# Kernel tuning notes

Hardware: AMD Instinct MI355X
Metric: run time of the kernel (lower is better)

The kernel has to match this reference:

```python
import math
import jax, jax.numpy as jnp
import numpy as np

B, L, D, DK = 2, 2046, 1024, 64
H, GH, LH = 16, 8, 8   # total / global / local heads
WS = 3                  # hardcoded window_size in source
MAX_VAL = 1e9


def setup_inputs() -> dict:
    key = jax.random.key(0)
    ks = jax.random.split(key, 7)
    x = jax.random.normal(ks[0], (B, L, D), dtype=jnp.float32)
    mask = jnp.ones((B, 1, L, L), dtype=jnp.float32)
    s = 0.02
    Wq = jax.random.normal(ks[1], (D, D), dtype=jnp.float32) * s   # torch Linear weight [out,in]
    bq = jnp.zeros((D,), dtype=jnp.float32)
    Wk = jax.random.normal(ks[2], (H, DK, DK), dtype=jnp.float32) * s
    bk = jnp.zeros((H, DK), dtype=jnp.float32)
    Wv = jax.random.normal(ks[3], (H, DK, DK), dtype=jnp.float32) * s
    bv = jnp.zeros((H, DK), dtype=jnp.float32)
    return {"x": x, "mask": mask, "Wq": Wq, "bq": bq,
            "Wk": Wk, "bk": bk, "Wv": Wv, "bv": bv}


def reference(x, mask, Wq, bq, Wk, bk, Wv, bv):
    b, l, d = x.shape
    scale = 1.0 / math.sqrt(DK)

    q = x @ Wq.T + bq                                   # [b,l,d]
    q = q.reshape(b, l, H, DK).transpose(0, 2, 1, 3)    # [b,h,l,dk]
    kv = x.reshape(b, l, H, DK).transpose(0, 2, 1, 3)   # k and v are both raw x

    # ---------------- global heads: full attention ----------------
    qg = q[:, :GH]                                      # [b,gh,l,dk]
    kg = kv[:, :GH]
    kgp = jnp.einsum('bhli,hoi->bhlo', kg, Wk[:GH]) + bk[:GH][None, :, None, :]
    vgp = jnp.einsum('bhli,hoi->bhlo', kg, Wv[:GH]) + bv[:GH][None, :, None, :]
    sg = jnp.einsum('bhld,bhmd->bhlm', qg, kgp) * scale  # [b,gh,l,l]
    mfull = (mask[:, 0] == 0)[:, None]                   # [b,1,l,l]
    sg = jnp.where(mfull, -MAX_VAL, sg)
    pg = jax.nn.softmax(sg, axis=-1)
    vg = jnp.einsum('bhlm,bhmd->bhld', pg, vgp)          # [b,gh,l,dk]

    # ---------------- local heads: window-pooled attention ----------------
    nw = l // WS
    ql = q[:, GH:]                                       # [b,lh,l,dk]
    kl = kv[:, GH:]
    # mean-pool keys over non-overlapping windows (pool_method='mean');
    # source uses the SAME pooled tensor for both K and V (repeat(2,...))
    kw = kl.reshape(b, LH, nw, WS, DK).mean(axis=3)      # [b,lh,nw,dk]
    # window mask: majority of window columns valid, per query row
    wm = mask[:, 0].reshape(b, l, nw, WS).sum(-1) >= math.ceil(WS / 2)  # [b,l,nw]
    klp = jnp.einsum('bhni,hoi->bhno', kw, Wk[GH:]) + bk[GH:][None, :, None, :]
    vlp = jnp.einsum('bhni,hoi->bhno', kw, Wv[GH:]) + bv[GH:][None, :, None, :]
    sl = jnp.einsum('bhld,bhnd->bhln', ql, klp) * scale  # [b,lh,l,nw]
    sl = jnp.where(~wm[:, None], -MAX_VAL, sl)
    pl = jax.nn.softmax(sl, axis=-1)
    vl = jnp.einsum('bhln,bhnd->bhld', pl, vlp)          # [b,lh,l,dk]

    value_all = jnp.concatenate([vg, vl], axis=1)        # [b,h,l,dk]
    return (value_all, pg, pl)
```

## Files before the change

kernel.cpp:

```cpp
#include <hip/hip_runtime.h>
#include <hip/hip_bf16.h>
#include <stdint.h>

typedef __bf16 bf16;
typedef bf16 bf16x8 __attribute__((ext_vector_type(8)));
typedef float f32x4 __attribute__((ext_vector_type(4)));

#define B_ 2
#define L_ 2046
#define H_ 16
#define NW_ 682
#define LP_ 2048
#define NWP_ 704
#define M_ (B_*L_)
#define SCALE_ 0.125f

__device__ inline bf16x8 zf8() {
  bf16x8 v;
#pragma unroll
  for (int e = 0; e < 8; ++e) v[e] = (bf16)0.0f;
  return v;
}

__device__ inline uint32_t pkbf(float a, float b) {
  uint16_t ua = __builtin_bit_cast(uint16_t, (bf16)a);
  uint16_t ub = __builtin_bit_cast(uint16_t, (bf16)b);
  return (uint32_t)ua | ((uint32_t)ub << 16);
}
__device__ inline float upk_lo(uint32_t u) { return __builtin_bit_cast(float, u << 16); }
__device__ inline float upk_hi(uint32_t u) { return __builtin_bit_cast(float, u & 0xffff0000u); }

__global__ __launch_bounds__(256) void cast4(const float* __restrict__ in,
                                             bf16* __restrict__ out, int n) {
  int i = (blockIdx.x * 256 + threadIdx.x) * 4;
  if (i + 3 < n) {
    float4 v = *reinterpret_cast<const float4*>(in + i);
    bf16 tmp[4];
    tmp[0] = (bf16)v.x; tmp[1] = (bf16)v.y; tmp[2] = (bf16)v.z; tmp[3] = (bf16)v.w;
    *reinterpret_cast<uint64_t*>(out + i) = *reinterpret_cast<const uint64_t*>(tmp);
  } else {
    for (; i < n; ++i) out[i] = (bf16)in[i];
  }
}

__global__ __launch_bounds__(256) void qgemm_t(const bf16* __restrict__ X,
                                               const bf16* __restrict__ W,
                                               const float* __restrict__ bq,
                                               bf16* __restrict__ Q) {
  __shared__ bf16 As[64 * 40];
  __shared__ bf16 Bs[128 * 40];
  int t = threadIdx.x, lane = t & 63, w = t >> 6;
  int lid = lane & 15, g = lane >> 4;
  int m0 = blockIdx.x * 64, n0 = blockIdx.y * 128;
  int wm = (w >> 1) * 32, wn = (w & 1) * 64;
  f32x4 z4 = {0.f, 0.f, 0.f, 0.f};
  f32x4 acc[2][4];
#pragma unroll
  for (int mi = 0; mi < 2; ++mi)
#pragma unroll
    for (int ni = 0; ni < 4; ++ni) acc[mi][ni] = z4;
  int r1 = t >> 2, c1 = t & 3;
  for (int k0 = 0; k0 < 1024; k0 += 32) {
    int ga = m0 + r1; if (ga >= M_) ga = M_ - 1;
    bf16x8 av = *reinterpret_cast<const bf16x8*>(X + (size_t)ga * 1024 + k0 + c1 * 8);
    bf16x8 bv1 = *reinterpret_cast<const bf16x8*>(W + (size_t)(n0 + r1) * 1024 + k0 + c1 * 8);
    bf16x8 bv2 = *reinterpret_cast<const bf16x8*>(W + (size_t)(n0 + 64 + r1) * 1024 + k0 + c1 * 8);
    __syncthreads();
    *reinterpret_cast<bf16x8*>(As + r1 * 40 + c1 * 8) = av;
    *reinterpret_cast<bf16x8*>(Bs + r1 * 40 + c1 * 8) = bv1;
    *reinterpret_cast<bf16x8*>(Bs + (64 + r1) * 40 + c1 * 8) = bv2;
    __syncthreads();
    bf16x8 af[2], bfr[4];
#pragma unroll
    for (int mi = 0; mi < 2; ++mi)
      af[mi] = *reinterpret_cast<const bf16x8*>(As + (wm + mi * 16 + lid) * 40 + g * 8);
#pragma unroll
    for (int ni = 0; ni < 4; ++ni)
      bfr[ni] = *reinterpret_cast<const bf16x8*>(Bs + (wn + ni * 16 + lid) * 40 + g * 8);
#pragma unroll
    for (int mi = 0; mi < 2; ++mi)
#pragma unroll
      for (int ni = 0; ni < 4; ++ni)
        acc[mi][ni] = __builtin_amdgcn_mfma_f32_16x16x32_bf16(af[mi], bfr[ni], acc[mi][ni], 0, 0, 0);
  }
  float bias[4];
#pragma unroll
  for (int ni = 0; ni < 4; ++ni) bias[ni] = bq[n0 + wn + ni * 16 + lid];
#pragma unroll
  for (int mi = 0; mi < 2; ++mi)
#pragma unroll
    for (int r = 0; r < 4; ++r) {
      int row = m0 + wm + mi * 16 + g * 4 + r;
      if (row < M_) {
#pragma unroll
        for (int ni = 0; ni < 4; ++ni)
          Q[(size_t)row * 1024 + n0 + wn + ni * 16 + lid] = (bf16)(acc[mi][ni][r] + bias[ni]);
      }
    }
}

__global__ __launch_bounds__(256) void proj_g32(const float* __restrict__ x,
    const float* __restrict__ Wk, const float* __restrict__ bk,
    const float* __restrict__ Wv, const float* __restrict__ bv,
    bf16* __restrict__ KGP, bf16* __restrict__ VGT) {
  __shared__ float xs[64][64];
  __shared__ float wks[64][65];
  __shared__ float wvs[64][65];
  int t = threadIdx.x;
  int lb = blockIdx.x, bh = blockIdx.y;
  int b = bh >> 3, h = bh & 7;
  int l0 = lb * 64;
  for (int idx = t; idx < 4096; idx += 256) {
    int r = idx >> 6, c = idx & 63;
    int l = l0 + r;
    xs[r][c] = (l < L_) ? x[((size_t)b * L_ + l) * 1024 + h * 64 + c] : 0.0f;
    wks[r][c] = Wk[(size_t)h * 4096 + idx];
    wvs[r][c] = Wv[(size_t)h * 4096 + idx];
  }
  __syncthreads();
  int o = t & 63, lg = t >> 6;
  float kbias = bk[h * 64 + o], vbias = bv[h * 64 + o];
  float vacc[16];
  const size_t outb = (size_t)bh * LP_ * 64;
  for (int ls = 0; ls < 16; ++ls) {
    int l = lg * 16 + ls;
    float ka = kbias, va = vbias;
#pragma unroll
    for (int i = 0; i < 64; ++i) {
      float xv = xs[l][i];
      ka = fmaf(xv, wks[o][i], ka);
      va = fmaf(xv, wvs[o][i], va);
    }
    KGP[outb + (size_t)(l0 + l) * 64 + o] = (bf16)ka;
    vacc[ls] = va;
  }
  __syncthreads();
#pragma unroll
  for (int ls = 0; ls < 16; ++ls) wvs[o][lg * 16 + ls] = vacc[ls];
  __syncthreads();
  for (int idx = t; idx < 4096; idx += 256) {
    int oo = idx >> 6, ll = idx & 63;
    VGT[(size_t)bh * 64 * LP_ + (size_t)oo * LP_ + l0 + ll] = (bf16)wvs[oo][ll];
  }
}

__global__ __launch_bounds__(256) void proj_l32(const float* __restrict__ x,
    const float* __restrict__ Wk, const float* __restrict__ bk,
    const float* __restrict__ Wv, const float* __restrict__ bv,
    bf16* __restrict__ KLP, bf16* __restrict__ VLT) {
  __shared__ float xs[64][64];
  __shared__ float wks[64][65];
  __shared__ float wvs[64][65];
  int t = threadIdx.x;
  int nb = blockIdx.x, bh = blockIdx.y;
  int b = bh >> 3, h = bh & 7;
  int n0 = nb * 64;
  int hh = 8 + h;
  for (int idx = t; idx < 4096; idx += 256) {
    int r = idx >> 6, c = idx & 63;
    int n = n0 + r;
    float v = 0.0f;
    if (n < NW_) {
      size_t base = ((size_t)b * L_ + 3 * n) * 1024 + hh * 64 + c;
      v = (x[base] + x[base + 1024] + x[base + 2048]) * (1.0f / 3.0f);
    }
    xs[r][c] = v;
    wks[r][c] = Wk[(size_t)hh * 4096 + idx];
    wvs[r][c] = Wv[(size_t)hh * 4096 + idx];
  }
  __syncthreads();
  int o = t & 63, lg = t >> 6;
  float kbias = bk[hh * 64 + o], vbias = bv[hh * 64 + o];
  float vacc[16];
  const size_t outb = (size_t)bh * NWP_ * 64;
  for (int ls = 0; ls < 16; ++ls) {
    int l = lg * 16 + ls;
    float ka = kbias, va = vbias;
#pragma unroll
    for (int i = 0; i < 64; ++i) {
      float xv = xs[l][i];
      ka = fmaf(xv, wks[o][i], ka);
      va = fmaf(xv, wvs[o][i], va);
    }
    KLP[outb + (size_t)(n0 + l) * 64 + o] = (bf16)ka;
    vacc[ls] = va;
  }
  __syncthreads();
#pragma unroll
  for (int ls = 0; ls < 16; ++ls) wvs[o][lg * 16 + ls] = vacc[ls];
  __syncthreads();
  for (int idx = t; idx < 4096; idx += 256) {
    int oo = idx >> 6, ll = idx & 63;
    VLT[(size_t)bh * 64 * NWP_ + (size_t)oo * NWP_ + n0 + ll] = (bf16)wvs[oo][ll];
  }
}

__global__ __launch_bounds__(256) void maskprep(const float* __restrict__ mask,
                                                uint64_t* __restrict__ gm,
                                                uint64_t* __restrict__ wm) {
  int row = blockIdx.x * 4 + (threadIdx.x >> 6);
  int lane = threadIdx.x & 63;
  if (row >= B_ * L_) return;
  int b = row / L_, l = row % L_;
  const float* mr = mask + (size_t)b * L_ * L_ + (size_t)l * L_;
  for (int w = 0; w < 32; ++w) {
    int m = w * 64 + lane;
    bool masked = (m >= L_) ? true : (mr[m] == 0.0f);
    uint64_t bal = __ballot(masked);
    if (lane == 0) gm[(size_t)row * 32 + w] = bal;
  }
  for (int w = 0; w < 11; ++w) {
    int n = w * 64 + lane;
    bool lmask = true;
    if (n < NW_) {
      float s = mr[3 * n] + mr[3 * n + 1] + mr[3 * n + 2];
      lmask = !(s >= 2.0f);
    }
    uint64_t bal = __ballot(lmask);
    if (lane == 0) wm[(size_t)row * 11 + w] = bal;
  }
}

__global__ __launch_bounds__(512, 2) void attn_gf(const bf16* __restrict__ Q,
    const bf16* __restrict__ K, const bf16* __restrict__ VT,
    const uint64_t* __restrict__ GM,
    float* __restrict__ OP, float* __restrict__ OV) {
  __shared__ float sums[128];
  __shared__ float strip2[2][16][257];
  int t = threadIdx.x;
  int lane = t & 63, wave = t >> 6;
  int lid = lane & 15, g = lane >> 4;
  int q0 = blockIdx.x * 16;
  int bh = blockIdx.y;
  int b = bh >> 3, h = bh & 7;
  const bf16* qb = Q + (size_t)b * L_ * 1024 + h * 64;
  const bf16* kb = K + (size_t)bh * LP_ * 64;
  const bf16* vtg = VT + (size_t)bh * 64 * LP_;
  const uint64_t* gmb = GM + (size_t)b * L_ * 32;

  bf16x8 aq0 = zf8(), aq1 = zf8();
  {
    int qr = q0 + lid;
    if (qr < L_) {
      aq0 = *reinterpret_cast<const bf16x8*>(qb + (size_t)qr * 1024 + g * 8);
      aq1 = *reinterpret_cast<const bf16x8*>(qb + (size_t)qr * 1024 + 32 + g * 8);
    }
  }
  uint32_t preg[32];
  float rs[4] = {0.f, 0.f, 0.f, 0.f};
#pragma unroll
  for (int it = 0; it < 8; ++it) {
    int p = it * 8 + wave;
    int c0 = p * 32;
    int col0 = c0 + lid, col1 = c0 + 16 + lid;
    bf16x8 bka0 = *reinterpret_cast<const bf16x8*>(kb + (size_t)col0 * 64 + g * 8);
    bf16x8 bka1 = *reinterpret_cast<const bf16x8*>(kb + (size_t)col0 * 64 + 32 + g * 8);
    bf16x8 bkb0 = *reinterpret_cast<const bf16x8*>(kb + (size_t)col1 * 64 + g * 8);
    bf16x8 bkb1 = *reinterpret_cast<const bf16x8*>(kb + (size_t)col1 * 64 + 32 + g * 8);
    f32x4 acc0 = {0.f, 0.f, 0.f, 0.f}, acc1 = {0.f, 0.f, 0.f, 0.f};
    acc0 = __builtin_amdgcn_mfma_f32_16x16x32_bf16(aq0, bka0, acc0, 0, 0, 0);
    acc0 = __builtin_amdgcn_mfma_f32_16x16x32_bf16(aq1, bka1, acc0, 0, 0, 0);
    acc1 = __builtin_amdgcn_mfma_f32_16x16x32_bf16(aq0, bkb0, acc1, 0, 0, 0);
    acc1 = __builtin_amdgcn_mfma_f32_16x16x32_bf16(aq1, bkb1, acc1, 0, 0, 0);
    int wi = c0 >> 6;
    int bit0 = c0 & 32;
#pragma unroll
    for (int r = 0; r < 4; ++r) {
      int qr = q0 + g * 4 + r;
      uint64_t w = (qr < L_) ? gmb[(size_t)qr * 32 + wi] : ~0ull;
      float pv0 = ((w >> (bit0 + lid)) & 1) ? 0.0f : __expf(acc0[r] * SCALE_);
      float pv1 = ((w >> (bit0 + 16 + lid)) & 1) ? 0.0f : __expf(acc1[r] * SCALE_);
      rs[r] += pv0 + pv1;
      preg[it * 4 + r] = pkbf(pv0, pv1);
    }
  }
#pragma unroll
  for (int off = 8; off >= 1; off >>= 1)
#pragma unroll
    for (int r = 0; r < 4; ++r) rs[r] += __shfl_xor(rs[r], off, 64);
  if (lid == 0) {
#pragma unroll
    for (int r = 0; r < 4; ++r) sums[wave * 16 + g * 4 + r] = rs[r];
  }
  __syncthreads();
  float invr[4];
#pragma unroll
  for (int r = 0; r < 4; ++r) {
    int row = g * 4 + r;
    float s = 0.f;
#pragma unroll
    for (int ww = 0; ww < 8; ++ww) s += sums[ww * 16 + row];
    invr[r] = (s > 0.f) ? 1.0f / s : 0.0f;
  }
  int orow = t >> 5;
  int qrT = q0 + orow;
  bool rowok = (qrT < L_);
  const size_t rowb = (size_t)bh * L_ * L_ + (size_t)(rowok ? qrT : 0) * L_;
  int c8 = (t & 31) * 8;
  f32x4 vacc[4];
  f32x4 z4 = {0.f, 0.f, 0.f, 0.f};
#pragma unroll
  for (int dg = 0; dg < 4; ++dg) vacc[dg] = z4;
#pragma unroll
  for (int it = 0; it < 8; ++it) {
    float* sbuf = &strip2[it & 1][0][0];
    int mb0 = it * 256;
#pragma unroll
    for (int r = 0; r < 4; ++r) {
      uint32_t u = preg[it * 4 + r];
      sbuf[(g * 4 + r) * 257 + wave * 32 + lid] = upk_lo(u) * invr[r];
      sbuf[(g * 4 + r) * 257 + wave * 32 + 16 + lid] = upk_hi(u) * invr[r];
    }
    __syncthreads();
    int col = mb0 + c8;
    if (rowok) {
#pragma unroll
      for (int pr = 0; pr < 4; ++pr) {
        int cc = c8 + pr * 2;
        if (col + pr * 2 + 1 < L_) {
          float2 o2 = make_float2(sbuf[orow * 257 + cc], sbuf[orow * 257 + cc + 1]);
          *reinterpret_cast<float2*>(OP + rowb + col + pr * 2) = o2;
        }
      }
    }
    bf16x8 af;
#pragma unroll
    for (int e = 0; e < 8; ++e) af[e] = (bf16)sbuf[lid * 257 + wave * 32 + g * 8 + e];
#pragma unroll
    for (int dg = 0; dg < 4; ++dg) {
      bf16x8 bv8 = *reinterpret_cast<const bf16x8*>(vtg + (size_t)(dg * 16 + lid) * LP_ + mb0 + wave * 32 + g * 8);
      vacc[dg] = __builtin_amdgcn_mfma_f32_16x16x32_bf16(af, bv8, vacc[dg], 0, 0, 0);
    }
  }
  __syncthreads();
  float* red = &strip2[0][0][0];
#pragma unroll
  for (int wsel = 0; wsel < 8; ++wsel) {
    if (wave == wsel) {
#pragma unroll
      for (int dg = 0; dg < 4; ++dg)
#pragma unroll
        for (int r = 0; r < 4; ++r) {
          if (wsel == 0) red[(g * 4 + r) * 257 + dg * 16 + lid] = vacc[dg][r];
          else           red[(g * 4 + r) * 257 + dg * 16 + lid] += vacc[dg][r];
        }
    }
    __syncthreads();
  }
  float* ob = OV + (((size_t)b * 16 + h) * L_) * 64;
  for (int idx = t; idx < 1024; idx += 512) {
    int r = idx >> 6, d = idx & 63;
    int qr = q0 + r;
    if (qr < L_) ob[(size_t)qr * 64 + d] = red[r * 257 + d];
  }
}

__global__ __launch_bounds__(512, 2) void attn_lf(const bf16* __restrict__ Q,
    const bf16* __restrict__ K, const bf16* __restrict__ VT,
    const uint64_t* __restrict__ WM,
    float* __restrict__ OP, float* __restrict__ OV) {
  __shared__ float sums[128];
  __shared__ float strip2[2][16][257];
  int t = threadIdx.x;
  int lane = t & 63, wave = t >> 6;
  int lid = lane & 15, g = lane >> 4;
  int q0 = blockIdx.x * 16;
  int bh = blockIdx.y;
  int b = bh >> 3, h = bh & 7;
  const bf16* qb = Q + (size_t)b * L_ * 1024 + (8 + h) * 64;
  const bf16* kb = K + (size_t)bh * NWP_ * 64;
  const bf16* vtg = VT + (size_t)bh * 64 * NWP_;
  const uint64_t* wmb = WM + (size_t)b * L_ * 11;

  bf16x8 aq0 = zf8(), aq1 = zf8();
  {
    int qr = q0 + lid;
    if (qr < L_) {
      aq0 = *reinterpret_cast<const bf16x8*>(qb + (size_t)qr * 1024 + g * 8);
      aq1 = *reinterpret_cast<const bf16x8*>(qb + (size_t)qr * 1024 + 32 + g * 8);
    }
  }
  uint32_t preg[12];
  float rs[4] = {0.f, 0.f, 0.f, 0.f};
#pragma unroll
  for (int it = 0; it < 3; ++it) {
    int p = it * 8 + wave;
    if (p < 22) {
      int c0 = p * 32;
      int col0 = c0 + lid, col1 = c0 + 16 + lid;
      bf16x8 bka0 = *reinterpret_cast<const bf16x8*>(kb + (size_t)col0 * 64 + g * 8);
      bf16x8 bka1 = *reinterpret_cast<const bf16x8*>(kb + (size_t)col0 * 64 + 32 + g * 8);
      bf16x8 bkb0 = *reinterpret_cast<const bf16x8*>(kb + (size_t)col1 * 64 + g * 8);
      bf16x8 bkb1 = *reinterpret_cast<const bf16x8*>(kb + (size_t)col1 * 64 + 32 + g * 8);
      f32x4 acc0 = {0.f, 0.f, 0.f, 0.f}, acc1 = {0.f, 0.f, 0.f, 0.f};
      acc0 = __builtin_amdgcn_mfma_f32_16x16x32_bf16(aq0, bka0, acc0, 0, 0, 0);
      acc0 = __builtin_amdgcn_mfma_f32_16x16x32_bf16(aq1, bka1, acc0, 0, 0, 0);
      acc1 = __builtin_amdgcn_mfma_f32_16x16x32_bf16(aq0, bkb0, acc1, 0, 0, 0);
      acc1 = __builtin_amdgcn_mfma_f32_16x16x32_bf16(aq1, bkb1, acc1, 0, 0, 0);
      int wi = c0 >> 6;
      int bit0 = c0 & 32;
#pragma unroll
      for (int r = 0; r < 4; ++r) {
        int qr = q0 + g * 4 + r;
        uint64_t w = (qr < L_) ? wmb[(size_t)qr * 11 + wi] : ~0ull;
        float pv0 = ((w >> (bit0 + lid)) & 1) ? 0.0f : __expf(acc0[r] * SCALE_);
        float pv1 = ((w >> (bit0 + 16 + lid)) & 1) ? 0.0f : __expf(acc1[r] * SCALE_);
        rs[r] += pv0 + pv1;
        preg[it * 4 + r] = pkbf(pv0, pv1);
      }
    }
  }
#pragma unroll
  for (int off = 8; off >= 1; off >>= 1)
#pragma unroll
    for (int r = 0; r < 4; ++r) rs[r] += __shfl_xor(rs[r], off, 64);
  if (lid == 0) {
#pragma unroll
    for (int r = 0; r < 4; ++r) sums[wave * 16 + g * 4 + r] = rs[r];
  }
  __syncthreads();
  float invr[4];
#pragma unroll
  for (int r = 0; r < 4; ++r) {
    int row = g * 4 + r;
    float s = 0.f;
#pragma unroll
    for (int ww = 0; ww < 8; ++ww) s += sums[ww * 16 + row];
    invr[r] = (s > 0.f) ? 1.0f / s : 0.0f;
  }
  int orow = t >> 5;
  int qrT = q0 + orow;
  bool rowok = (qrT < L_);
  const size_t rowb = (size_t)bh * L_ * NW_ + (size_t)(rowok ? qrT : 0) * NW_;
  int c8 = (t & 31) * 8;
  f32x4 vacc[4];
  f32x4 z4 = {0.f, 0.f, 0.f, 0.f};
#pragma unroll
  for (int dg = 0; dg < 4; ++dg) vacc[dg] = z4;
#pragma unroll
  for (int it = 0; it < 3; ++it) {
    float* sbuf = &strip2[it & 1][0][0];
    int p = it * 8 + wave;
    bool act = (p < 22);
    int mb0 = it * 256;
    if (act) {
#pragma unroll
      for (int r = 0; r < 4; ++r) {
        uint32_t u = preg[it * 4 + r];
        sbuf[(g * 4 + r) * 257 + wave * 32 + lid] = upk_lo(u) * invr[r];
        sbuf[(g * 4 + r) * 257 + wave * 32 + 16 + lid] = upk_hi(u) * invr[r];
      }
    }
    __syncthreads();
    int col = mb0 + c8;
    if (rowok) {
#pragma unroll
      for (int pr = 0; pr < 4; ++pr) {
        int cc = c8 + pr * 2;
        if (col + pr * 2 + 1 < NW_) {
          float2 o2 = make_float2(sbuf[orow * 257 + cc], sbuf[orow * 257 + cc + 1]);
          *reinterpret_cast<float2*>(OP + rowb + col + pr * 2) = o2;
        }
      }
    }
    if (act) {
      bf16x8 af;
#pragma unroll
      for (int e = 0; e < 8; ++e) af[e] = (bf16)sbuf[lid * 257 + wave * 32 + g * 8 + e];
#pragma unroll
      for (int dg = 0; dg < 4; ++dg) {
        bf16x8 bv8 = *reinterpret_cast<const bf16x8*>(vtg + (size_t)(dg * 16 + lid) * NWP_ + mb0 + wave * 32 + g * 8);
        vacc[dg] = __builtin_amdgcn_mfma_f32_16x16x32_bf16(af, bv8, vacc[dg], 0, 0, 0);
      }
    }
  }
  __syncthreads();
  float* red = &strip2[0][0][0];
#pragma unroll
  for (int wsel = 0; wsel < 8; ++wsel) {
    if (wave == wsel) {
#pragma unroll
      for (int dg = 0; dg < 4; ++dg)
#pragma unroll
        for (int r = 0; r < 4; ++r) {
          if (wsel == 0) red[(g * 4 + r) * 257 + dg * 16 + lid] = vacc[dg][r];
          else           red[(g * 4 + r) * 257 + dg * 16 + lid] += vacc[dg][r];
        }
    }
    __syncthreads();
  }
  float* ob = OV + (((size_t)b * 16 + 8 + h) * L_) * 64;
  for (int idx = t; idx < 1024; idx += 512) {
    int r = idx >> 6, d = idx & 63;
    int qr = q0 + r;
    if (qr < L_) ob[(size_t)qr * 64 + d] = red[r * 257 + d];
  }
}

extern "C" void kernel_launch(void* const* d_in, const int* in_sizes, int n_in,
                              void* d_out, int out_size, void* d_ws, size_t ws_size,
                              hipStream_t stream) {
  (void)in_sizes; (void)n_in; (void)out_size; (void)ws_size;
  const float* x    = (const float*)d_in[0];
  const float* mask = (const float*)d_in[1];
  const float* Wq   = (const float*)d_in[2];
  const float* bq   = (const float*)d_in[3];
  const float* Wk   = (const float*)d_in[4];
  const float* bk   = (const float*)d_in[5];
  const float* Wv   = (const float*)d_in[6];
  const float* bv   = (const float*)d_in[7];

  char* ws = (char*)d_ws;
  bf16* qbb     = (bf16*)(ws + 0);
  bf16* kgb     = (bf16*)(ws + 8380416);
  bf16* vgT     = (bf16*)(ws + 12574720);
  bf16* klb     = (bf16*)(ws + 16769024);
  bf16* vlT     = (bf16*)(ws + 18210816);
  uint64_t* gm  = (uint64_t*)(ws + 19652608);
  uint64_t* wm  = (uint64_t*)(ws + 20700160);
  bf16* xbb     = (bf16*)(ws + 21060256);
  bf16* wqb     = (bf16*)(ws + 29440672);

  float* out    = (float*)d_out;
  float* o_vall = out;
  float* o_pg   = out + 4190208;
  float* o_pl   = out + 71168064;

  cast4<<<4092, 256, 0, stream>>>(x, xbb, 4190208);
  cast4<<<1024, 256, 0, stream>>>(Wq, wqb, 1048576);
  qgemm_t<<<dim3(64, 8), 256, 0, stream>>>(xbb, wqb, bq, qbb);
  proj_g32<<<dim3(32, 16), 256, 0, stream>>>(x, Wk, bk, Wv, bv, kgb, vgT);
  proj_l32<<<dim3(11, 16), 256, 0, stream>>>(x, Wk, bk, Wv, bv, klb, vlT);
  maskprep<<<1023, 256, 0, stream>>>(mask, gm, wm);

  attn_gf<<<dim3(128, 16), 512, 0, stream>>>(qbb, kgb, vgT, gm, o_pg, o_vall);
  attn_lf<<<dim3(128, 16), 512, 0, stream>>>(qbb, klb, vlT, wm, o_pl, o_vall);
}
```

Measured before the change: 392.9 us.

## Use 1024-thread blocks with 16 waves, single-strip staging and tree reduction

Both attention kernels now run 16 waves per block instead of 8, so each wave handles fewer column tiles and keeps half as many packed probabilities in registers. The double-buffered 256-column staging strip is replaced by one 512-column strip, and each wave writes its own query row of probabilities. The serial eight-step cross-wave reduction of the PV accumulators becomes a log-depth tree reduction through shared memory, and wave 0 writes the output directly. This aims to raise occupancy and cut synchronisation steps, at the cost of a larger block and a second barrier in every iteration.

```diff
diff --git a/kernel.cpp b/kernel.cpp
--- a/kernel.cpp
+++ b/kernel.cpp
@@ -14,6 +14,9 @@
 #define NWP_ 704
 #define M_ (B_*L_)
 #define SCALE_ 0.125f
+#define STR 517
+#define RSTR 68
+#define RW (16*RSTR)
 
 __device__ inline bf16x8 zf8() {
   bf16x8 v;
@@ -221,12 +224,12 @@
   }
 }
 
-__global__ __launch_bounds__(512, 2) void attn_gf(const bf16* __restrict__ Q,
+__global__ __launch_bounds__(1024, 4) void attn_gf(const bf16* __restrict__ Q,
     const bf16* __restrict__ K, const bf16* __restrict__ VT,
     const uint64_t* __restrict__ GM,
     float* __restrict__ OP, float* __restrict__ OV) {
-  __shared__ float sums[128];
-  __shared__ float strip2[2][16][257];
+  __shared__ float sums[256];
+  __shared__ float pool[8704];
   int t = threadIdx.x;
   int lane = t & 63, wave = t >> 6;
   int lid = lane & 15, g = lane >> 4;
@@ -246,11 +249,11 @@
       aq1 = *reinterpret_cast<const bf16x8*>(qb + (size_t)qr * 1024 + 32 + g * 8);
     }
   }
-  uint32_t preg[32];
+  uint32_t preg[16];
   float rs[4] = {0.f, 0.f, 0.f, 0.f};
 #pragma unroll
-  for (int it = 0; it < 8; ++it) {
-    int p = it * 8 + wave;
+  for (int it = 0; it < 4; ++it) {
+    int p = it * 16 + wave;
     int c0 = p * 32;
     int col0 = c0 + lid, col1 = c0 + 16 + lid;
     bf16x8 bka0 = *reinterpret_cast<const bf16x8*>(kb + (size_t)col0 * 64 + g * 8);
@@ -289,78 +292,84 @@
     int row = g * 4 + r;
     float s = 0.f;
 #pragma unroll
-    for (int ww = 0; ww < 8; ++ww) s += sums[ww * 16 + row];
+    for (int ww = 0; ww < 16; ++ww) s += sums[ww * 16 + row];
     invr[r] = (s > 0.f) ? 1.0f / s : 0.0f;
   }
-  int orow = t >> 5;
-  int qrT = q0 + orow;
-  bool rowok = (qrT < L_);
-  const size_t rowb = (size_t)bh * L_ * L_ + (size_t)(rowok ? qrT : 0) * L_;
-  int c8 = (t & 31) * 8;
   f32x4 vacc[4];
   f32x4 z4 = {0.f, 0.f, 0.f, 0.f};
 #pragma unroll
   for (int dg = 0; dg < 4; ++dg) vacc[dg] = z4;
-#pragma unroll
-  for (int it = 0; it < 8; ++it) {
-    float* sbuf = &strip2[it & 1][0][0];
-    int mb0 = it * 256;
+  int qrW = q0 + wave;
+  bool rowokW = (qrW < L_);
+  const size_t rowbW = (size_t)bh * L_ * L_ + (size_t)(rowokW ? qrW : 0) * L_;
+#pragma unroll
+  for (int it = 0; it < 4; ++it) {
+    int mb0 = it * 512;
 #pragma unroll
     for (int r = 0; r < 4; ++r) {
       uint32_t u = preg[it * 4 + r];
-      sbuf[(g * 4 + r) * 257 + wave * 32 + lid] = upk_lo(u) * invr[r];
-      sbuf[(g * 4 + r) * 257 + wave * 32 + 16 + lid] = upk_hi(u) * invr[r];
-    }
-    __syncthreads();
-    int col = mb0 + c8;
-    if (rowok) {
-#pragma unroll
-      for (int pr = 0; pr < 4; ++pr) {
-        int cc = c8 + pr * 2;
-        if (col + pr * 2 + 1 < L_) {
-          float2 o2 = make_float2(sbuf[orow * 257 + cc], sbuf[orow * 257 + cc + 1]);
-          *reinterpret_cast<float2*>(OP + rowb + col + pr * 2) = o2;
-        }
-      }
-    }
+      pool[(g * 4 + r) * STR + wave * 32 + lid] = upk_lo(u) * invr[r];
+      pool[(g * 4 + r) * STR + wave * 32 + 16 + lid] = upk_hi(u) * invr[r];
+    }
+    __syncthreads();
     bf16x8 af;
 #pragma unroll
-    for (int e = 0; e < 8; ++e) af[e] = (bf16)sbuf[lid * 257 + wave * 32 + g * 8 + e];
+    for (int e = 0; e < 8; ++e) af[e] = (bf16)pool[lid * STR + wave * 32 + g * 8 + e];
 #pragma unroll
     for (int dg = 0; dg < 4; ++dg) {
       bf16x8 bv8 = *reinterpret_cast<const bf16x8*>(vtg + (size_t)(dg * 16 + lid) * LP_ + mb0 + wave * 32 + g * 8);
       vacc[dg] = __builtin_amdgcn_mfma_f32_16x16x32_bf16(af, bv8, vacc[dg], 0, 0, 0);
     }
-  }
-  __syncthreads();
-  float* red = &strip2[0][0][0];
-#pragma unroll
-  for (int wsel = 0; wsel < 8; ++wsel) {
-    if (wave == wsel) {
+    if (rowokW) {
+#pragma unroll
+      for (int seg = 0; seg < 4; ++seg) {
+        int cc = seg * 128 + lane * 2;
+        int col = mb0 + cc;
+        if (col + 1 < L_) {
+          float2 o2 = make_float2(pool[wave * STR + cc], pool[wave * STR + cc + 1]);
+          *reinterpret_cast<float2*>(OP + rowbW + col) = o2;
+        }
+      }
+    }
+    __syncthreads();
+  }
+#pragma unroll
+  for (int s = 8; s >= 1; s >>= 1) {
+    if (wave >= s && wave < 2 * s) {
 #pragma unroll
       for (int dg = 0; dg < 4; ++dg)
 #pragma unroll
-        for (int r = 0; r < 4; ++r) {
-          if (wsel == 0) red[(g * 4 + r) * 257 + dg * 16 + lid] = vacc[dg][r];
-          else           red[(g * 4 + r) * 257 + dg * 16 + lid] += vacc[dg][r];
-        }
-    }
-    __syncthreads();
-  }
-  float* ob = OV + (((size_t)b * 16 + h) * L_) * 64;
-  for (int idx = t; idx < 1024; idx += 512) {
-    int r = idx >> 6, d = idx & 63;
-    int qr = q0 + r;
-    if (qr < L_) ob[(size_t)qr * 64 + d] = red[r * 257 + d];
-  }
-}
-
-__global__ __launch_bounds__(512, 2) void attn_lf(const bf16* __restrict__ Q,
+        for (int r = 0; r < 4; ++r)
+          pool[(wave - s) * RW + (g * 4 + r) * RSTR + dg * 16 + lid] = vacc[dg][r];
+    }
+    __syncthreads();
+    if (wave < s) {
+#pragma unroll
+      for (int dg = 0; dg < 4; ++dg)
+#pragma unroll
+        for (int r = 0; r < 4; ++r)
+          vacc[dg][r] += pool[wave * RW + (g * 4 + r) * RSTR + dg * 16 + lid];
+    }
+    __syncthreads();
+  }
+  if (wave == 0) {
+    float* ob = OV + (((size_t)b * 16 + h) * L_) * 64;
+#pragma unroll
+    for (int dg = 0; dg < 4; ++dg)
+#pragma unroll
+      for (int r = 0; r < 4; ++r) {
+        int qr = q0 + g * 4 + r;
+        if (qr < L_) ob[(size_t)qr * 64 + dg * 16 + lid] = vacc[dg][r];
+      }
+  }
+}
+
+__global__ __launch_bounds__(1024, 4) void attn_lf(const bf16* __restrict__ Q,
     const bf16* __restrict__ K, const bf16* __restrict__ VT,
     const uint64_t* __restrict__ WM,
     float* __restrict__ OP, float* __restrict__ OV) {
-  __shared__ float sums[128];
-  __shared__ float strip2[2][16][257];
+  __shared__ float sums[256];
+  __shared__ float pool[8704];
   int t = threadIdx.x;
   int lane = t & 63, wave = t >> 6;
   int lid = lane & 15, g = lane >> 4;
@@ -380,11 +389,11 @@
       aq1 = *reinterpret_cast<const bf16x8*>(qb + (size_t)qr * 1024 + 32 + g * 8);
     }
   }
-  uint32_t preg[12];
+  uint32_t preg[8];
   float rs[4] = {0.f, 0.f, 0.f, 0.f};
 #pragma unroll
-  for (int it = 0; it < 3; ++it) {
-    int p = it * 8 + wave;
+  for (int it = 0; it < 2; ++it) {
+    int p = it * 16 + wave;
     if (p < 22) {
       int c0 = p * 32;
       int col0 = c0 + lid, col1 = c0 + 16 + lid;
@@ -425,75 +434,81 @@
     int row = g * 4 + r;
     float s = 0.f;
 #pragma unroll
-    for (int ww = 0; ww < 8; ++ww) s += sums[ww * 16 + row];
+    for (int ww = 0; ww < 16; ++ww) s += sums[ww * 16 + row];
     invr[r] = (s > 0.f) ? 1.0f / s : 0.0f;
   }
-  int orow = t >> 5;
-  int qrT = q0 + orow;
-  bool rowok = (qrT < L_);
-  const size_t rowb = (size_t)bh * L_ * NW_ + (size_t)(rowok ? qrT : 0) * NW_;
-  int c8 = (t & 31) * 8;
   f32x4 vacc[4];
   f32x4 z4 = {0.f, 0.f, 0.f, 0.f};
 #pragma unroll
   for (int dg = 0; dg < 4; ++dg) vacc[dg] = z4;
-#pragma unroll
-  for (int it = 0; it < 3; ++it) {
-    float* sbuf = &strip2[it & 1][0][0];
-    int p = it * 8 + wave;
+  int qrW = q0 + wave;
+  bool rowokW = (qrW < L_);
+  const size_t rowbW = (size_t)bh * L_ * NW_ + (size_t)(rowokW ? qrW : 0) * NW_;
+#pragma unroll
+  for (int it = 0; it < 2; ++it) {
+    int p = it * 16 + wave;
     bool act = (p < 22);
-    int mb0 = it * 256;
+    int mb0 = it * 512;
     if (act) {
 #pragma unroll
       for (int r = 0; r < 4; ++r) {
         uint32_t u = preg[it * 4 + r];
-        sbuf[(g * 4 + r) * 257 + wave * 32 + lid] = upk_lo(u) * invr[r];
-        sbuf[(g * 4 + r) * 257 + wave * 32 + 16 + lid] = upk_hi(u) * invr[r];
-      }
-    }
-    __syncthreads();
-    int col = mb0 + c8;
-    if (rowok) {
-#pragma unroll
-      for (int pr = 0; pr < 4; ++pr) {
-        int cc = c8 + pr * 2;
-        if (col + pr * 2 + 1 < NW_) {
-          float2 o2 = make_float2(sbuf[orow * 257 + cc], sbuf[orow * 257 + cc + 1]);
-          *reinterpret_cast<float2*>(OP + rowb + col + pr * 2) = o2;
-        }
-      }
-    }
+        pool[(g * 4 + r) * STR + wave * 32 + lid] = upk_lo(u) * invr[r];
+        pool[(g * 4 + r) * STR + wave * 32 + 16 + lid] = upk_hi(u) * invr[r];
+      }
+    }
+    __syncthreads();
     if (act) {
       bf16x8 af;
 #pragma unroll
-      for (int e = 0; e < 8; ++e) af[e] = (bf16)sbuf[lid * 257 + wave * 32 + g * 8 + e];
+      for (int e = 0; e < 8; ++e) af[e] = (bf16)pool[lid * STR + wave * 32 + g * 8 + e];
 #pragma unroll
       for (int dg = 0; dg < 4; ++dg) {
         bf16x8 bv8 = *reinterpret_cast<const bf16x8*>(vtg + (size_t)(dg * 16 + lid) * NWP_ + mb0 + wave * 32 + g * 8);
         vacc[dg] = __builtin_amdgcn_mfma_f32_16x16x32_bf16(af, bv8, vacc[dg], 0, 0, 0);
       }
     }
-  }
-  __syncthreads();
-  float* red = &strip2[0][0][0];
-#pragma unroll
-  for (int wsel = 0; wsel < 8; ++wsel) {
-    if (wave == wsel) {
+    if (rowokW) {
+#pragma unroll
+      for (int seg = 0; seg < 4; ++seg) {
+        int cc = seg * 128 + lane * 2;
+        int col = mb0 + cc;
+        if (col + 1 < NW_) {
+          float2 o2 = make_float2(pool[wave * STR + cc], pool[wave * STR + cc + 1]);
+          *reinterpret_cast<float2*>(OP + rowbW + col) = o2;
+        }
+      }
+    }
+    __syncthreads();
+  }
+#pragma unroll
+  for (int s = 8; s >= 1; s >>= 1) {
+    if (wave >= s && wave < 2 * s) {
 #pragma unroll
       for (int dg = 0; dg < 4; ++dg)
 #pragma unroll
-        for (int r = 0; r < 4; ++r) {
-          if (wsel == 0) red[(g * 4 + r) * 257 + dg * 16 + lid] = vacc[dg][r];
-          else           red[(g * 4 + r) * 257 + dg * 16 + lid] += vacc[dg][r];
-        }
-    }
-    __syncthreads();
-  }
-  float* ob = OV + (((size_t)b * 16 + 8 + h) * L_) * 64;
-  for (int idx = t; idx < 1024; idx += 512) {
-    int r = idx >> 6, d = idx & 63;
-    int qr = q0 + r;
-    if (qr < L_) ob[(size_t)qr * 64 + d] = red[r * 257 + d];
+        for (int r = 0; r < 4; ++r)
+          pool[(wave - s) * RW + (g * 4 + r) * RSTR + dg * 16 + lid] = vacc[dg][r];
+    }
+    __syncthreads();
+    if (wave < s) {
+#pragma unroll
+      for (int dg = 0; dg < 4; ++dg)
+#pragma unroll
+        for (int r = 0; r < 4; ++r)
+          vacc[dg][r] += pool[wave * RW + (g * 4 + r) * RSTR + dg * 16 + lid];
+    }
+    __syncthreads();
+  }
+  if (wave == 0) {
+    float* ob = OV + (((size_t)b * 16 + 8 + h) * L_) * 64;
+#pragma unroll
+    for (int dg = 0; dg < 4; ++dg)
+#pragma unroll
+      for (int r = 0; r < 4; ++r) {
+        int qr = q0 + g * 4 + r;
+        if (qr < L_) ob[(size_t)qr * 64 + dg * 16 + lid] = vacc[dg][r];
+      }
   }
 }
 
@@ -533,6 +548,6 @@
   proj_l32<<<dim3(11, 16), 256, 0, stream>>>(x, Wk, bk, Wv, bv, klb, vlT);
   maskprep<<<1023, 256, 0, stream>>>(mask, gm, wm);
 
-  attn_gf<<<dim3(128, 16), 512, 0, stream>>>(qbb, kgb, vgT, gm, o_pg, o_vall);
-  attn_lf<<<dim3(128, 16), 512, 0, stream>>>(qbb, klb, vlT, wm, o_pl, o_vall);
-}
+  attn_gf<<<dim3(128, 16), 1024, 0, stream>>>(qbb, kgb, vgT, gm, o_pg, o_vall);
+  attn_lf<<<dim3(128, 16), 1024, 0, stream>>>(qbb, klb, vlT, wm, o_pl, o_vall);
+}
```

Result: no change. 386.6 us (-1.6%).
